# Performance work log

Measured on AMD Instinct MI355X. Metric: run time of the kernel, lower is better.

Reference implementation:

```python
import jax, jax.numpy as jnp
import numpy as np

B, T, D, H, L, DFF, MAXLEN = 4, 2048, 512, 8, 6, 2048, 2048
DK = D // H
SCALE = float(1.0 / np.sqrt(DK * 2))  # 1/sqrt(d_k*2)


def layer_norm(x, g, b, eps=1e-5):
    m = jnp.mean(x, axis=-1, keepdims=True)
    v = jnp.var(x, axis=-1, keepdims=True)
    return (x - m) / jnp.sqrt(v + eps) * g + b


def setup_inputs() -> dict:
    key = jax.random.key(0)
    it = iter(jax.random.split(key, 48))
    def n(shape, std=0.02):
        return jax.random.normal(next(it), shape, dtype=jnp.float32) * std
    inp = {}
    inp['x'] = jax.random.normal(next(it), (B, T), dtype=jnp.float32)
    inp['ip_w'] = n((1, D)); inp['ip_b'] = jnp.zeros((D,))
    inp['ip_ln_g'] = jnp.ones((D,)); inp['ip_ln_b'] = jnp.zeros((D,))
    inp['pos_embed'] = n((MAXLEN, D), 0.01)
    inp['pad_token'] = n((D,), 0.01)
    inp['Wq'] = n((L, D, D)); inp['bq'] = jnp.zeros((L, D))
    inp['Wk'] = n((L, D, D)); inp['bk'] = jnp.zeros((L, D))
    inp['Wv'] = n((L, D, D)); inp['bv'] = jnp.zeros((L, D))
    inp['Wo'] = n((L, D, D)); inp['bo'] = jnp.zeros((L, D))
    inp['ln1_g'] = jnp.ones((L, D)); inp['ln1_b'] = jnp.zeros((L, D))
    inp['ln2_g'] = jnp.ones((L, D)); inp['ln2_b'] = jnp.zeros((L, D))
    inp['W1'] = n((L, D, DFF)); inp['b1'] = jnp.zeros((L, DFF))
    inp['W2'] = n((L, DFF, D)); inp['b2'] = jnp.zeros((L, D))
    inp['gate1'] = jnp.full((L,), 0.1); inp['gate2'] = jnp.full((L,), 0.1)
    inp['fn_g'] = jnp.ones((D,)); inp['fn_b'] = jnp.zeros((D,))
    for p in ['bh', 'ah', 'ch']:
        inp[p + '_ln_g'] = jnp.ones((D,)); inp[p + '_ln_b'] = jnp.zeros((D,))
    inp['bh_w'] = n((D, 2), 0.01); inp['bh_b'] = jnp.zeros((2,))
    inp['ah_w'] = n((D, 1), 0.01); inp['ah_b'] = jnp.zeros((1,))
    inp['ch_w'] = n((D, 1), 0.01); inp['ch_b'] = jnp.zeros((1,))
    return inp


def _forward(x, ip_w, ip_b, ip_ln_g, ip_ln_b, pos_embed, pad_token,
             Wq, bq, Wk, bk, Wv, bv, Wo, bo,
             ln1_g, ln1_b, ln2_g, ln2_b, W1, b1, W2, b2, gate1, gate2,
             fn_g, fn_b, bh_ln_g, bh_ln_b, bh_w, bh_b,
             ah_ln_g, ah_ln_b, ah_w, ah_b, ch_ln_g, ch_ln_b, ch_w, ch_b):
    Bx, Tx = x.shape
    xc = jnp.clip(x, -10.0, 10.0)
    pad_mask = xc == -1.0  # [B,T]
    h = layer_norm(xc[..., None] @ ip_w + ip_b, ip_ln_g, ip_ln_b)  # [B,T,D]
    h = h + 0.1 * pos_embed[None, :Tx, :]
    h = jnp.where(pad_mask[..., None], pad_token, h)
    cmask = jnp.triu(jnp.full((Tx, Tx), -10000.0, dtype=h.dtype), k=1)  # additive causal mask
    for i in range(L):
        xn = layer_norm(h, ln1_g[i], ln1_b[i])
        def heads(w, b, xn=xn):
            return (xn @ w + b).reshape(Bx, Tx, H, DK).transpose(0, 2, 1, 3)
        q = heads(Wq[i], bq[i]); k = heads(Wk[i], bk[i]); v = heads(Wv[i], bv[i])
        q = q / jnp.maximum(jnp.linalg.norm(q, axis=-1, keepdims=True), 1e-8)
        k = k / jnp.maximum(jnp.linalg.norm(k, axis=-1, keepdims=True), 1e-8)
        scores = jnp.clip(jnp.einsum('bhtd,bhsd->bhts', q, k) * SCALE, -5.0, 5.0) + cmask
        a = jax.nn.softmax(scores / 1.5, axis=-1)
        o = jnp.einsum('bhts,bhsd->bhtd', a, v).transpose(0, 2, 1, 3).reshape(Bx, Tx, D)
        h = h + gate1[i] * ((o @ Wo[i] + bo[i]) * 0.5)
        xn2 = layer_norm(h, ln2_g[i], ln2_b[i])
        ffn = jax.nn.gelu(xn2 @ W1[i] + b1[i], approximate=False) @ W2[i] + b2[i]
        h = jnp.clip(h + gate2[i] * ffn, -10.0, 10.0)
    h = layer_norm(h, fn_g, fn_b)
    m = (~pad_mask).astype(h.dtype)[..., None]
    mean = (h * m).sum(axis=1) / jnp.maximum(m.sum(axis=1), 1.0)  # masked mean pool [B,D]
    binary = layer_norm(mean, bh_ln_g, bh_ln_b) @ bh_w + bh_b
    anomaly = layer_norm(mean, ah_ln_g, ah_ln_b) @ ah_w + ah_b
    caustic = jax.nn.sigmoid(layer_norm(mean, ch_ln_g, ch_ln_b) @ ch_w + ch_b)
    return jnp.concatenate([binary, anomaly, caustic], axis=-1)  # [B,4]


def reference(x, ip_w, ip_b, ip_ln_g, ip_ln_b, pos_embed, pad_token,
              Wq, bq, Wk, bk, Wv, bv, Wo, bo,
              ln1_g, ln1_b, ln2_g, ln2_b, W1, b1, W2, b2, gate1, gate2,
              fn_g, fn_b, bh_ln_g, bh_ln_b, bh_w, bh_b,
              ah_ln_g, ah_ln_b, ah_w, ah_b, ch_ln_g, ch_ln_b, ch_w, ch_b):
    return _forward(x, ip_w, ip_b, ip_ln_g, ip_ln_b, pos_embed, pad_token,
                    Wq, bq, Wk, bk, Wv, bv, Wo, bo,
                    ln1_g, ln1_b, ln2_g, ln2_b, W1, b1, W2, b2, gate1, gate2,
                    fn_g, fn_b, bh_ln_g, bh_ln_b, bh_w, bh_b,
                    ah_ln_g, ah_ln_b, ah_w, ah_b, ch_ln_g, ch_ln_b, ch_w, ch_b)
```

## Files before the change

kernel.cpp:

```cpp
#include <hip/hip_runtime.h>
#include <hip/hip_bf16.h>
#include <math.h>

constexpr int Bsz = 4, T = 2048, D = 512, H = 8, Lnum = 6, DFF = 2048, DK = 64;
constexpr int QS2 = 1024;
constexpr float K2 = 0.08838834764831845f / 1.5f;

typedef __attribute__((ext_vector_type(8))) short svec8;
typedef __attribute__((ext_vector_type(4))) float fvec4;

__device__ __forceinline__ fvec4 mfma16(svec8 a, svec8 b, fvec4 c) {
    return __builtin_amdgcn_mfma_f32_16x16x32_bf16(a, b, c, 0, 0, 0);
}
__device__ __forceinline__ unsigned short f2b(float f) {
    unsigned int u = __float_as_uint(f);
    u += 0x7fffu + ((u >> 16) & 1u);
    return (unsigned short)(u >> 16);
}
__device__ __forceinline__ unsigned int pk2b(float a, float b) {
    __hip_bfloat162 h = __float22bfloat162_rn(float2{a, b});
    return *(unsigned int*)&h;
}
__device__ __forceinline__ float wave_red_sum(float v) {
    for (int o = 32; o > 0; o >>= 1) v += __shfl_down(v, o, 64);
    return __shfl(v, 0, 64);
}
__device__ __forceinline__ void glds16(const unsigned short* g, unsigned short* l) {
    __builtin_amdgcn_global_load_lds(
        (const __attribute__((address_space(1))) unsigned int*)g,
        (__attribute__((address_space(3))) unsigned int*)l, 16, 0, 0);
}
#define FRAG(buf, row, kq) (*(const svec8*)((buf) + (((row) << 6) | ((((kq) ^ ((row) & 7))) << 3))))

__global__ __launch_bounds__(64)
void embed_kernel(const float* __restrict__ x, const float* __restrict__ ip_w,
                  const float* __restrict__ ip_b, const float* __restrict__ g,
                  const float* __restrict__ bta, const float* __restrict__ pos,
                  const float* __restrict__ pad_tok, float* __restrict__ h)
{
    int row = blockIdx.x;
    int t = row & (T - 1);
    int lane = threadIdx.x;
    float xv = x[row];
    float xc = fminf(fmaxf(xv, -10.f), 10.f);
    bool pad = (xc == -1.0f);
    float pre[8];
    float s = 0.f, s2 = 0.f;
#pragma unroll
    for (int j = 0; j < 8; j++) {
        int d = j * 64 + lane;
        float p = xc * ip_w[d] + ip_b[d];
        pre[j] = p; s += p; s2 += p * p;
    }
    s = wave_red_sum(s); s2 = wave_red_sum(s2);
    float m = s * (1.f / 512.f);
    float var = s2 * (1.f / 512.f) - m * m;
    float rstd = 1.f / sqrtf(var + 1e-5f);
#pragma unroll
    for (int j = 0; j < 8; j++) {
        int d = j * 64 + lane;
        float hv = (pre[j] - m) * rstd * g[d] + bta[d] + 0.1f * pos[(size_t)t * D + d];
        if (pad) hv = pad_tok[d];
        h[(size_t)row * D + d] = hv;
    }
}

__global__ __launch_bounds__(256)
void ln_kernel(const float* __restrict__ in, float* __restrict__ out,
               const float* __restrict__ g, const float* __restrict__ b)
{
    int row = blockIdx.x * 4 + (threadIdx.x >> 6);
    int lane = threadIdx.x & 63;
    const float* r = in + (size_t)row * D;
    float4 v0 = ((const float4*)r)[lane];
    float4 v1 = ((const float4*)r)[lane + 64];
    float s = v0.x + v0.y + v0.z + v0.w + v1.x + v1.y + v1.z + v1.w;
    float s2 = v0.x*v0.x + v0.y*v0.y + v0.z*v0.z + v0.w*v0.w
             + v1.x*v1.x + v1.y*v1.y + v1.z*v1.z + v1.w*v1.w;
    s = wave_red_sum(s); s2 = wave_red_sum(s2);
    float m = s * (1.f / 512.f);
    float var = s2 * (1.f / 512.f) - m * m;
    float rstd = 1.f / sqrtf(var + 1e-5f);
    float4 g0 = ((const float4*)g)[lane], g1 = ((const float4*)g)[lane + 64];
    float4 b0 = ((const float4*)b)[lane], b1 = ((const float4*)b)[lane + 64];
    float4 o0, o1;
    o0.x = (v0.x - m) * rstd * g0.x + b0.x; o0.y = (v0.y - m) * rstd * g0.y + b0.y;
    o0.z = (v0.z - m) * rstd * g0.z + b0.z; o0.w = (v0.w - m) * rstd * g0.w + b0.w;
    o1.x = (v1.x - m) * rstd * g1.x + b1.x; o1.y = (v1.y - m) * rstd * g1.y + b1.y;
    o1.z = (v1.z - m) * rstd * g1.z + b1.z; o1.w = (v1.w - m) * rstd * g1.w + b1.w;
    ((float4*)(out + (size_t)row * D))[lane] = o0;
    ((float4*)(out + (size_t)row * D))[lane + 64] = o1;
}

__global__ __launch_bounds__(256)
void ln_bf16_kernel(const float* __restrict__ in, unsigned short* __restrict__ out,
                    const float* __restrict__ g, const float* __restrict__ b)
{
    int row = blockIdx.x * 4 + (threadIdx.x >> 6);
    int lane = threadIdx.x & 63;
    const float* r = in + (size_t)row * D;
    float4 v0 = ((const float4*)r)[lane];
    float4 v1 = ((const float4*)r)[lane + 64];
    float s = v0.x + v0.y + v0.z + v0.w + v1.x + v1.y + v1.z + v1.w;
    float s2 = v0.x*v0.x + v0.y*v0.y + v0.z*v0.z + v0.w*v0.w
             + v1.x*v1.x + v1.y*v1.y + v1.z*v1.z + v1.w*v1.w;
    s = wave_red_sum(s); s2 = wave_red_sum(s2);
    float m = s * (1.f / 512.f);
    float var = s2 * (1.f / 512.f) - m * m;
    float rstd = 1.f / sqrtf(var + 1e-5f);
    float4 g0 = ((const float4*)g)[lane], g1 = ((const float4*)g)[lane + 64];
    float4 b0 = ((const float4*)b)[lane], b1 = ((const float4*)b)[lane + 64];
    unsigned short o0[4], o1[4];
    o0[0] = f2b((v0.x - m) * rstd * g0.x + b0.x); o0[1] = f2b((v0.y - m) * rstd * g0.y + b0.y);
    o0[2] = f2b((v0.z - m) * rstd * g0.z + b0.z); o0[3] = f2b((v0.w - m) * rstd * g0.w + b0.w);
    o1[0] = f2b((v1.x - m) * rstd * g1.x + b1.x); o1[1] = f2b((v1.y - m) * rstd * g1.y + b1.y);
    o1[2] = f2b((v1.z - m) * rstd * g1.z + b1.z); o1[3] = f2b((v1.w - m) * rstd * g1.w + b1.w);
    *(uint2*)(out + (size_t)row * D + lane * 4) = *(uint2*)o0;
    *(uint2*)(out + (size_t)row * D + 256 + lane * 4) = *(uint2*)o1;
}

__global__ __launch_bounds__(256)
void wconv_kernel(const float* __restrict__ wq, const float* __restrict__ wk,
                  const float* __restrict__ wv, const float* __restrict__ wo,
                  const float* __restrict__ w1, const float* __restrict__ w2,
                  unsigned short* __restrict__ oq, unsigned short* __restrict__ ok,
                  unsigned short* __restrict__ ov, unsigned short* __restrict__ oo,
                  unsigned short* __restrict__ o1, unsigned short* __restrict__ o2)
{
    __shared__ float tile[32][33];
    int bid = blockIdx.x;
    const float* in; unsigned short* out; int K, N, kt, nt;
    if (bid < 1024) {
        int sel = bid >> 8, loc = bid & 255;
        in  = sel == 0 ? wq : sel == 1 ? wk : sel == 2 ? wv : wo;
        out = sel == 0 ? oq : sel == 1 ? ok : sel == 2 ? ov : oo;
        K = 512; N = 512; kt = loc >> 4; nt = loc & 15;
    } else if (bid < 2048) {
        int loc = bid - 1024; in = w1; out = o1; K = 512; N = 2048; kt = loc >> 6; nt = loc & 63;
    } else {
        int loc = bid - 2048; in = w2; out = o2; K = 2048; N = 512; kt = loc >> 4; nt = loc & 15;
    }
    int k0 = kt * 32, n0 = nt * 32;
    int t = threadIdx.x;
    int kr = t >> 3, nc = (t & 7) * 4;
    float4 v = *(const float4*)(in + (size_t)(k0 + kr) * N + n0 + nc);
    tile[kr][nc] = v.x; tile[kr][nc + 1] = v.y; tile[kr][nc + 2] = v.z; tile[kr][nc + 3] = v.w;
    __syncthreads();
    unsigned short o[4];
#pragma unroll
    for (int i = 0; i < 4; i++) o[i] = f2b(tile[nc + i][kr]);
    *(uint2*)(out + (size_t)(n0 + kr) * K + k0 + nc) = *(uint2*)o;
}

template<int EPI, int OBF, int BM>
__global__ __launch_bounds__(256)
void gemm_bf16(const unsigned short* __restrict__ A, const unsigned short* __restrict__ BT,
               const float* __restrict__ bias, const float* __restrict__ bias_b,
               const float* __restrict__ bias_c, const float* __restrict__ res,
               void* __restrict__ Cv, unsigned short* __restrict__ vtout,
               int M, int N, int K, const float* __restrict__ gate_p)
{
    constexpr int WN = (BM == 128) ? 2 : 4;
    constexpr int WSPAN = 128 / WN;
    constexpr int NT = WSPAN / 16;
    constexpr int MT = 4;
    constexpr int ACALLS = BM / 32;
    constexpr int SMEMSZ = (EPI == 0) ? 17408 : (BM * 64 + 128 * 64);
    __shared__ __align__(16) unsigned short SMEM[SMEMSZ];
    unsigned short* As = SMEM;
    unsigned short* Bs = SMEM + BM * 64;
    const int tid = threadIdx.x, w = tid >> 6, lane = tid & 63, quad = lane >> 4, ln = lane & 15;
    const int wm = w / WN, wn = w % WN;
    const int m0 = blockIdx.x * BM, n0 = blockIdx.y * 128;
    const int jg = (lane & 7) ^ ((lane >> 3) & 7);
    const int rb = w * 8 + (lane >> 3);
    const unsigned short* Agl = A + (size_t)(m0 + rb) * K + jg * 8;
    const unsigned short* Bgl = BT + (size_t)(n0 + rb) * K + jg * 8;

    fvec4 acc[MT][NT];
#pragma unroll
    for (int mt = 0; mt < MT; mt++)
#pragma unroll
        for (int nt = 0; nt < NT; nt++)
#pragma unroll
            for (int r = 0; r < 4; r++) acc[mt][nt][r] = 0.f;

    for (int k0 = 0; k0 < K; k0 += 64) {
        __syncthreads();
#pragma unroll
        for (int c = 0; c < ACALLS; c++)
            glds16(Agl + k0 + (size_t)c * 32 * K, As + c * 2048 + w * 512);
#pragma unroll
        for (int c = 0; c < 4; c++)
            glds16(Bgl + k0 + (size_t)c * 32 * K, Bs + c * 2048 + w * 512);
        __syncthreads();
#pragma unroll
        for (int kk = 0; kk < 2; kk++) {
            svec8 af[MT], bfr[NT];
#pragma unroll
            for (int mt = 0; mt < MT; mt++)
                af[mt] = FRAG(As, wm * 64 + mt * 16 + ln, kk * 4 + quad);
#pragma unroll
            for (int nt = 0; nt < NT; nt++)
                bfr[nt] = FRAG(Bs, wn * WSPAN + nt * 16 + ln, kk * 4 + quad);
#pragma unroll
            for (int mt = 0; mt < MT; mt++)
#pragma unroll
                for (int nt = 0; nt < NT; nt++)
                    acc[mt][nt] = mfma16(af[mt], bfr[nt], acc[mt][nt]);
        }
    }

    const float gate = (EPI == 1 || EPI == 3) ? gate_p[0] : 0.f;
    float bb[NT];
#pragma unroll
    for (int nt = 0; nt < NT; nt++) {
        int n = n0 + wn * WSPAN + nt * 16 + ln;
        if (EPI == 0) {
            int nseg = n >> 9;
            const float* bsel = nseg == 0 ? bias : (nseg == 1 ? bias_b : bias_c);
            bb[nt] = bsel[n - nseg * 512];
        } else {
            bb[nt] = bias[n];
        }
    }

    if (EPI == 0 && n0 >= 1024) {
        __syncthreads();
#pragma unroll
        for (int mt = 0; mt < MT; mt++) {
#pragma unroll
            for (int nt = 0; nt < NT; nt++) {
                int nl = wn * 64 + nt * 16 + ln;
                int mb = wm * 64 + mt * 16 + quad * 4;
                unsigned int lo = pk2b(acc[mt][nt][0] + bb[nt], acc[mt][nt][1] + bb[nt]);
                unsigned int hi = pk2b(acc[mt][nt][2] + bb[nt], acc[mt][nt][3] + bb[nt]);
                uint2 u; u.x = lo; u.y = hi;
                *(uint2*)(SMEM + nl * 136 + mb) = u;
            }
        }
        __syncthreads();
        int row = tid >> 1, half = (tid & 1) * 64;
        unsigned short* dst = vtout + ((size_t)((m0 >> 11) * 512 + (n0 - 1024) + row)) * T
                              + (m0 & (T - 1)) + half;
        const unsigned short* src = SMEM + row * 136 + half;
#pragma unroll
        for (int j = 0; j < 8; j++) *(uint4*)(dst + j * 8) = *(const uint4*)(src + j * 8);
        return;
    }

#pragma unroll
    for (int mt = 0; mt < MT; mt++) {
        float v[NT][4];
#pragma unroll
        for (int nt = 0; nt < NT; nt++)
#pragma unroll
            for (int r = 0; r < 4; r++) v[nt][r] = acc[mt][nt][r] + bb[nt];
        if (EPI == 0) {
            const float fac = ((n0 + wn * WSPAN) < 512) ? K2 : 1.f;
#pragma unroll
            for (int r = 0; r < 4; r++) {
                float s = 0.f;
#pragma unroll
                for (int nt = 0; nt < NT; nt++) s += v[nt][r] * v[nt][r];
                s += __shfl_xor(s, 1); s += __shfl_xor(s, 2);
                s += __shfl_xor(s, 4); s += __shfl_xor(s, 8);
                float rs = fac / fmaxf(sqrtf(s), 1e-8f);
#pragma unroll
                for (int nt = 0; nt < NT; nt++) v[nt][r] *= rs;
            }
        }
#pragma unroll
        for (int nt = 0; nt < NT; nt++) {
            int n = n0 + wn * WSPAN + nt * 16 + ln;
#pragma unroll
            for (int r = 0; r < 4; r++) {
                int m = m0 + wm * 64 + mt * 16 + quad * 4 + r;
                float val = v[nt][r];
                if (EPI == 0) {
                    ((unsigned short*)Cv)[(size_t)m * QS2 + n] = f2b(val);
                } else {
                    size_t off = (size_t)m * N + n;
                    if (EPI == 1) val = res[off] + gate * 0.5f * val;
                    else if (EPI == 2) {
                        float u = val;
                        float z = 0.7978845608028654f * fmaf(0.044715f * u, u * u, u);
                        float e = __builtin_amdgcn_exp2f(z * 2.8853900817779268f);
                        float rr = __builtin_amdgcn_rcpf(e + 1.f);
                        val = u * (1.f - rr);
                    }
                    else if (EPI == 3) val = fminf(fmaxf(res[off] + gate * val, -10.f), 10.f);
                    if (OBF) ((unsigned short*)Cv)[off] = f2b(val);
                    else ((float*)Cv)[off] = val;
                }
            }
        }
    }
}

template<bool DIAG>
__device__ __forceinline__ void attn_step(
    const unsigned short* Q, unsigned short* Ps, const unsigned short* Ks, const unsigned short* Vt,
    fvec4 (&oacc)[4], fvec4& lacc, int w, int quad, int ln)
{
    constexpr short BONE = (short)0x3F80;
    const svec8 ONES8 = {BONE, BONE, BONE, BONE, BONE, BONE, BONE, BONE};
    svec8 qf0 = FRAG(Q, w * 16 + ln, quad);
    svec8 qf1 = FRAG(Q, w * 16 + ln, 4 + quad);
    const int qrow = w * 16 + ln;
#pragma unroll
    for (int nt = 0; nt < 4; nt++) {
        fvec4 z; z[0] = z[1] = z[2] = z[3] = 0.f;
        z = mfma16(FRAG(Ks, nt * 16 + ln, quad), qf0, z);
        z = mfma16(FRAG(Ks, nt * 16 + ln, 4 + quad), qf1, z);
        const int sbase = nt * 16 + quad * 4;
        float p[4];
#pragma unroll
        for (int r = 0; r < 4; r++) {
            float y = z[r];
            float pv = fmaf(y, fmaf(y, 0.5f, 1.f), 1.f);
            if (DIAG && (sbase + r > qrow)) pv = 0.f;
            p[r] = pv;
        }
        uint2 u; u.x = pk2b(p[0], p[1]); u.y = pk2b(p[2], p[3]);
        int chunk = sbase >> 3, off = sbase & 7;
        *(uint2*)(Ps + ((qrow << 6) | ((chunk ^ (qrow & 7)) << 3) | off)) = u;
    }
#pragma unroll
    for (int ks = 0; ks < 2; ks++) {
        svec8 pa = FRAG(Ps, w * 16 + ln, ks * 4 + quad);
        lacc = mfma16(pa, ONES8, lacc);
#pragma unroll
        for (int nt = 0; nt < 4; nt++)
            oacc[nt] = mfma16(pa, FRAG(Vt, nt * 16 + ln, ks * 4 + quad), oacc[nt]);
    }
}

__global__ __launch_bounds__(256)
void attn_pair_kernel(const unsigned short* __restrict__ qkv, const unsigned short* __restrict__ vt,
                      unsigned short* __restrict__ o)
{
    __shared__ __align__(16) unsigned short QA[4096], QB[4096];
    __shared__ __align__(16) unsigned short K0[4096], V0[4096], K1[4096], V1[4096];
    __shared__ __align__(16) unsigned short Ps[4096];
    const int fid = blockIdx.x;
    const int xcd = fid & 7, slot = fid >> 3;
    const int bh = xcd * 4 + (slot & 3);
    const int p = slot >> 2;
    const int b = bh >> 3, hh = bh & 7;
    const int qtA = p, qtB = 31 - p, nst = 32 - p;
    const int tid = threadIdx.x, w = tid >> 6, lane = tid & 63, quad = lane >> 4, ln = lane & 15;
    const int rl = lane >> 3, sl = lane & 7, jgz = sl ^ rl;
    const int w8 = w * 8;
    const int grow = w8 + rl;
    const unsigned short* qrow_p = qkv + ((size_t)(b * T) + grow) * QS2 + hh * 64 + jgz * 8;
    const unsigned short* krow_p = qrow_p + 512;
    const unsigned short* vrow_p = vt + ((size_t)(bh * 64) + grow) * T + jgz * 8;

    glds16(qrow_p + (size_t)(qtA * 64) * QS2, QA + w8 * 64);
    glds16(qrow_p + (size_t)(qtA * 64 + 32) * QS2, QA + (w8 + 32) * 64);
    glds16(qrow_p + (size_t)(qtB * 64) * QS2, QB + w8 * 64);
    glds16(qrow_p + (size_t)(qtB * 64 + 32) * QS2, QB + (w8 + 32) * 64);

    fvec4 oA[4], oB[4], lAv, lBv;
#pragma unroll
    for (int r = 0; r < 4; r++) { lAv[r] = 0.f; lBv[r] = 0.f; }
#pragma unroll
    for (int nt = 0; nt < 4; nt++)
#pragma unroll
        for (int r = 0; r < 4; r++) { oA[nt][r] = 0.f; oB[nt][r] = 0.f; }

    const int Nph = (nst + 1) >> 1;
    for (int ph = 0; ph < Nph; ph++) {
        const int s0 = 2 * ph, s1 = 2 * ph + 1;
        __syncthreads();
        glds16(krow_p + (size_t)(s0 * 64) * QS2, K0 + w8 * 64);
        glds16(krow_p + (size_t)(s0 * 64 + 32) * QS2, K0 + (w8 + 32) * 64);
        glds16(vrow_p + s0 * 64, V0 + w8 * 64);
        glds16(vrow_p + (size_t)32 * T + s0 * 64, V0 + (w8 + 32) * 64);
        if (s1 < nst) {
            glds16(krow_p + (size_t)(s1 * 64) * QS2, K1 + w8 * 64);
            glds16(krow_p + (size_t)(s1 * 64 + 32) * QS2, K1 + (w8 + 32) * 64);
            glds16(vrow_p + s1 * 64, V1 + w8 * 64);
            glds16(vrow_p + (size_t)32 * T + s1 * 64, V1 + (w8 + 32) * 64);
        }
        __syncthreads();
        if (s0 == nst - 1) attn_step<true >(QB, Ps, K0, V0, oB, lBv, w, quad, ln);
        else               attn_step<false>(QB, Ps, K0, V0, oB, lBv, w, quad, ln);
        if (s0 <= p) {
            if (s0 == p) attn_step<true >(QA, Ps, K0, V0, oA, lAv, w, quad, ln);
            else         attn_step<false>(QA, Ps, K0, V0, oA, lAv, w, quad, ln);
        }
        if (s1 < nst) {
            if (s1 == nst - 1) attn_step<true >(QB, Ps, K1, V1, oB, lBv, w, quad, ln);
            else               attn_step<false>(QB, Ps, K1, V1, oB, lBv, w, quad, ln);
            if (s1 <= p) {
                if (s1 == p) attn_step<true >(QA, Ps, K1, V1, oA, lAv, w, quad, ln);
                else         attn_step<false>(QA, Ps, K1, V1, oA, lAv, w, quad, ln);
            }
        }
    }

    unsigned short* ogA = o + (size_t)(b * T + qtA * 64 + w * 16 + quad * 4) * D + hh * 64;
    unsigned short* ogB = o + (size_t)(b * T + qtB * 64 + w * 16 + quad * 4) * D + hh * 64;
#pragma unroll
    for (int r = 0; r < 4; r++) {
        float ia = 1.f / lAv[r], ib = 1.f / lBv[r];
#pragma unroll
        for (int nt = 0; nt < 4; nt++) {
            ogA[(size_t)r * D + nt * 16 + ln] = f2b(oA[nt][r] * ia);
            ogB[(size_t)r * D + nt * 16 + ln] = f2b(oB[nt][r] * ib);
        }
    }
}

__global__ __launch_bounds__(256)
void pool_kernel(const float* __restrict__ hn, const float* __restrict__ x, float* __restrict__ part)
{
    int b = blockIdx.x, ch = blockIdx.y, tid = threadIdx.x;
    int t0 = ch * 128;
    float s0 = 0.f, s1 = 0.f, cnt = 0.f;
    for (int tt = 0; tt < 128; tt++) {
        int t = t0 + tt;
        float xv = x[b * T + t];
        float m = (xv == -1.0f) ? 0.f : 1.f;
        cnt += m;
        const float* r = hn + ((size_t)(b * T + t)) * D;
        s0 += r[tid] * m;
        s1 += r[tid + 256] * m;
    }
    float* pr = part + (size_t)(b * 16 + ch) * 513;
    pr[tid] = s0; pr[tid + 256] = s1;
    if (tid == 0) pr[512] = cnt;
}

__global__ __launch_bounds__(64)
void head_kernel(const float* __restrict__ part,
                 const float* __restrict__ bh_g, const float* __restrict__ bh_bl,
                 const float* __restrict__ ah_g, const float* __restrict__ ah_bl,
                 const float* __restrict__ ch_g, const float* __restrict__ ch_bl,
                 const float* __restrict__ bh_w, const float* __restrict__ bh_b2,
                 const float* __restrict__ ah_w, const float* __restrict__ ah_b2,
                 const float* __restrict__ ch_w, const float* __restrict__ ch_b2,
                 float* __restrict__ out)
{
    int b = blockIdx.x, lane = threadIdx.x;
    float cnt = 0.f;
    for (int c = 0; c < 16; c++) cnt += part[(size_t)(b * 16 + c) * 513 + 512];
    float denom = fmaxf(cnt, 1.f);
    float md[8];
    float s = 0.f, s2 = 0.f;
#pragma unroll
    for (int j = 0; j < 8; j++) {
        int d = j * 64 + lane;
        float acc = 0.f;
        for (int c = 0; c < 16; c++) acc += part[(size_t)(b * 16 + c) * 513 + d];
        md[j] = acc / denom;
        s += md[j]; s2 += md[j] * md[j];
    }
    s = wave_red_sum(s); s2 = wave_red_sum(s2);
    float mu = s * (1.f / 512.f);
    float var = s2 * (1.f / 512.f) - mu * mu;
    float rstd = 1.f / sqrtf(var + 1e-5f);
    float a0 = 0.f, a1 = 0.f, a2 = 0.f, a3 = 0.f;
#pragma unroll
    for (int j = 0; j < 8; j++) {
        int d = j * 64 + lane;
        float z = (md[j] - mu) * rstd;
        float zb = z * bh_g[d] + bh_bl[d];
        a0 += zb * bh_w[d * 2 + 0];
        a1 += zb * bh_w[d * 2 + 1];
        a2 += (z * ah_g[d] + ah_bl[d]) * ah_w[d];
        a3 += (z * ch_g[d] + ch_bl[d]) * ch_w[d];
    }
    a0 = wave_red_sum(a0); a1 = wave_red_sum(a1);
    a2 = wave_red_sum(a2); a3 = wave_red_sum(a3);
    if (lane == 0) {
        out[b * 4 + 0] = a0 + bh_b2[0];
        out[b * 4 + 1] = a1 + bh_b2[1];
        out[b * 4 + 2] = a2 + ah_b2[0];
        float t3 = a3 + ch_b2[0];
        out[b * 4 + 3] = 1.f / (1.f + expf(-t3));
    }
}

extern "C" void kernel_launch(void* const* d_in, const int* in_sizes, int n_in,
                              void* d_out, int out_size, void* d_ws, size_t ws_size,
                              hipStream_t stream)
{
    const float* x      = (const float*)d_in[0];
    const float* ip_w   = (const float*)d_in[1];
    const float* ip_b   = (const float*)d_in[2];
    const float* ip_ln_g= (const float*)d_in[3];
    const float* ip_ln_b= (const float*)d_in[4];
    const float* pos    = (const float*)d_in[5];
    const float* pad_tok= (const float*)d_in[6];
    const float* Wq = (const float*)d_in[7];  const float* bq = (const float*)d_in[8];
    const float* Wk = (const float*)d_in[9];  const float* bk = (const float*)d_in[10];
    const float* Wv = (const float*)d_in[11]; const float* bv = (const float*)d_in[12];
    const float* Wo = (const float*)d_in[13]; const float* bo = (const float*)d_in[14];
    const float* ln1_g = (const float*)d_in[15]; const float* ln1_b = (const float*)d_in[16];
    const float* ln2_g = (const float*)d_in[17]; const float* ln2_b = (const float*)d_in[18];
    const float* W1 = (const float*)d_in[19]; const float* b1 = (const float*)d_in[20];
    const float* W2 = (const float*)d_in[21]; const float* b2 = (const float*)d_in[22];
    const float* gate1 = (const float*)d_in[23]; const float* gate2 = (const float*)d_in[24];
    const float* fn_g = (const float*)d_in[25]; const float* fn_b = (const float*)d_in[26];
    const float* bh_g  = (const float*)d_in[27]; const float* bh_bl = (const float*)d_in[28];
    const float* ah_g  = (const float*)d_in[29]; const float* ah_bl = (const float*)d_in[30];
    const float* ch_g  = (const float*)d_in[31]; const float* ch_bl = (const float*)d_in[32];
    const float* bh_w  = (const float*)d_in[33]; const float* bh_b2 = (const float*)d_in[34];
    const float* ah_w  = (const float*)d_in[35]; const float* ah_b2 = (const float*)d_in[36];
    const float* ch_w  = (const float*)d_in[37]; const float* ch_b2 = (const float*)d_in[38];

    char* ws = (char*)d_ws;
    float*          h     = (float*)ws;
    unsigned short* act_b = (unsigned short*)(ws + 16777216);
    unsigned short* qkv   = (unsigned short*)(ws + 25165824);
    unsigned short* mid_b = (unsigned short*)(ws + 41943040);
    float*          xn_f  = (float*)(ws + 41943040);
    unsigned short* wT    = (unsigned short*)(ws + 75497472);
    unsigned short* vt    = (unsigned short*)(ws + 81788928);
    float*          part  = (float*)(ws + 90177536);
    float*          out   = (float*)d_out;

    unsigned short* wqT = wT;
    unsigned short* wkT = wT + 262144;
    unsigned short* wvT = wT + 524288;
    unsigned short* woT = wT + 786432;
    unsigned short* w1T = wT + 1048576;
    unsigned short* w2T = wT + 2097152;

    embed_kernel<<<dim3(Bsz * T), dim3(64), 0, stream>>>(x, ip_w, ip_b, ip_ln_g, ip_ln_b, pos, pad_tok, h);

    for (int i = 0; i < Lnum; i++) {
        const size_t dd = (size_t)i * D * D;
        const size_t df = (size_t)i * D * DFF;
        wconv_kernel<<<dim3(3072), dim3(256), 0, stream>>>(Wq + dd, Wk + dd, Wv + dd, Wo + dd,
                                                           W1 + df, W2 + df,
                                                           wqT, wkT, wvT, woT, w1T, w2T);
        ln_bf16_kernel<<<dim3(Bsz * T / 4), dim3(256), 0, stream>>>(h, act_b, ln1_g + i * D, ln1_b + i * D);
        gemm_bf16<0, 1, 128><<<dim3(64, 12), dim3(256), 0, stream>>>(act_b, wqT, bq + i * D, bk + i * D, bv + i * D,
                                                                     nullptr, qkv, vt, Bsz * T, 1536, D, nullptr);
        attn_pair_kernel<<<dim3(512), dim3(256), 0, stream>>>(qkv, vt, act_b);
        gemm_bf16<1, 0, 64><<<dim3(128, 4), dim3(256), 0, stream>>>(act_b, woT, bo + i * D, nullptr, nullptr,
                                                                    h, h, nullptr, Bsz * T, D, D, gate1 + i);
        ln_bf16_kernel<<<dim3(Bsz * T / 4), dim3(256), 0, stream>>>(h, act_b, ln2_g + i * D, ln2_b + i * D);
        gemm_bf16<2, 1, 128><<<dim3(64, 16), dim3(256), 0, stream>>>(act_b, w1T, b1 + i * DFF, nullptr, nullptr,
                                                                     nullptr, mid_b, nullptr, Bsz * T, DFF, D, nullptr);
        gemm_bf16<3, 0, 64><<<dim3(128, 4), dim3(256), 0, stream>>>(mid_b, w2T, b2 + i * D, nullptr, nullptr,
                                                                    h, h, nullptr, Bsz * T, D, DFF, gate2 + i);
    }

    ln_kernel<<<dim3(Bsz * T / 4), dim3(256), 0, stream>>>(h, xn_f, fn_g, fn_b);
    pool_kernel<<<dim3(Bsz, 16), dim3(256), 0, stream>>>(xn_f, x, part);
    head_kernel<<<dim3(Bsz), dim3(64), 0, stream>>>(part, bh_g, bh_bl, ah_g, ah_bl, ch_g, ch_bl,
                                                    bh_w, bh_b2, ah_w, ah_b2, ch_w, ch_b2, out);
}
```

Before: 1.134 ms.

## Fuse LN1 into weight-conversion kernel and merge paired attention steps

The per-layer weight conversion and LN1 launches are folded into one prep kernel, with the extra blocks doing the layernorm rows, which removes one launch per layer. The attention kernel now keeps the Q fragments of both query tiles in registers after the first phase. It reuses the Q shared buffers as two P buffers and processes both tiles against each K/V tile in one merged step, so K and V fragments are loaded from LDS once. This cuts LDS reads and frees one 8KB buffer, but the fragments held for the whole loop raise register pressure.

Result: no change. 1.145 ms (+1.0%).

```diff
diff --git a/kernel.cpp b/kernel.cpp
--- a/kernel.cpp
+++ b/kernel.cpp
@@ -92,12 +92,10 @@
     ((float4*)(out + (size_t)row * D))[lane + 64] = o1;
 }
 
-__global__ __launch_bounds__(256)
-void ln_bf16_kernel(const float* __restrict__ in, unsigned short* __restrict__ out,
-                    const float* __restrict__ g, const float* __restrict__ b)
-{
-    int row = blockIdx.x * 4 + (threadIdx.x >> 6);
-    int lane = threadIdx.x & 63;
+__device__ __forceinline__ void ln_row_bf16(const float* __restrict__ in, unsigned short* __restrict__ out,
+                                            const float* __restrict__ g, const float* __restrict__ b,
+                                            int row, int lane)
+{
     const float* r = in + (size_t)row * D;
     float4 v0 = ((const float4*)r)[lane];
     float4 v1 = ((const float4*)r)[lane + 64];
@@ -120,15 +118,29 @@
 }
 
 __global__ __launch_bounds__(256)
-void wconv_kernel(const float* __restrict__ wq, const float* __restrict__ wk,
-                  const float* __restrict__ wv, const float* __restrict__ wo,
-                  const float* __restrict__ w1, const float* __restrict__ w2,
-                  unsigned short* __restrict__ oq, unsigned short* __restrict__ ok,
-                  unsigned short* __restrict__ ov, unsigned short* __restrict__ oo,
-                  unsigned short* __restrict__ o1, unsigned short* __restrict__ o2)
+void ln_bf16_kernel(const float* __restrict__ in, unsigned short* __restrict__ out,
+                    const float* __restrict__ g, const float* __restrict__ b)
+{
+    ln_row_bf16(in, out, g, b, blockIdx.x * 4 + (threadIdx.x >> 6), threadIdx.x & 63);
+}
+
+__global__ __launch_bounds__(256)
+void prep_kernel(const float* __restrict__ wq, const float* __restrict__ wk,
+                 const float* __restrict__ wv, const float* __restrict__ wo,
+                 const float* __restrict__ w1, const float* __restrict__ w2,
+                 unsigned short* __restrict__ oq, unsigned short* __restrict__ ok,
+                 unsigned short* __restrict__ ov, unsigned short* __restrict__ oo,
+                 unsigned short* __restrict__ o1, unsigned short* __restrict__ o2,
+                 const float* __restrict__ hin, unsigned short* __restrict__ lnout,
+                 const float* __restrict__ ln_g, const float* __restrict__ ln_b)
 {
     __shared__ float tile[32][33];
     int bid = blockIdx.x;
+    if (bid >= 3072) {
+        int row = (bid - 3072) * 4 + (threadIdx.x >> 6);
+        ln_row_bf16(hin, lnout, ln_g, ln_b, row, threadIdx.x & 63);
+        return;
+    }
     const float* in; unsigned short* out; int K, N, kt, nt;
     if (bid < 1024) {
         int sel = bid >> 8, loc = bid & 255;
@@ -298,41 +310,68 @@
     }
 }
 
-template<bool DIAG>
-__device__ __forceinline__ void attn_step(
-    const unsigned short* Q, unsigned short* Ps, const unsigned short* Ks, const unsigned short* Vt,
-    fvec4 (&oacc)[4], fvec4& lacc, int w, int quad, int ln)
+template<bool MERGED, bool DIAGS>
+__device__ __forceinline__ void attn_step2(
+    unsigned short* PsA, unsigned short* PsB,
+    const unsigned short* Ks, const unsigned short* Vt,
+    svec8 qA0, svec8 qA1, svec8 qB0, svec8 qB1,
+    bool diagA, bool diagB,
+    fvec4 (&oA)[4], fvec4& lA, fvec4 (&oB)[4], fvec4& lB,
+    int w, int quad, int ln)
 {
     constexpr short BONE = (short)0x3F80;
     const svec8 ONES8 = {BONE, BONE, BONE, BONE, BONE, BONE, BONE, BONE};
-    svec8 qf0 = FRAG(Q, w * 16 + ln, quad);
-    svec8 qf1 = FRAG(Q, w * 16 + ln, 4 + quad);
     const int qrow = w * 16 + ln;
+    const int prow_base = (qrow << 6);
 #pragma unroll
     for (int nt = 0; nt < 4; nt++) {
-        fvec4 z; z[0] = z[1] = z[2] = z[3] = 0.f;
-        z = mfma16(FRAG(Ks, nt * 16 + ln, quad), qf0, z);
-        z = mfma16(FRAG(Ks, nt * 16 + ln, 4 + quad), qf1, z);
+        svec8 kf0 = FRAG(Ks, nt * 16 + ln, quad);
+        svec8 kf1 = FRAG(Ks, nt * 16 + ln, 4 + quad);
         const int sbase = nt * 16 + quad * 4;
-        float p[4];
-#pragma unroll
-        for (int r = 0; r < 4; r++) {
-            float y = z[r];
-            float pv = fmaf(y, fmaf(y, 0.5f, 1.f), 1.f);
-            if (DIAG && (sbase + r > qrow)) pv = 0.f;
-            p[r] = pv;
-        }
-        uint2 u; u.x = pk2b(p[0], p[1]); u.y = pk2b(p[2], p[3]);
-        int chunk = sbase >> 3, off = sbase & 7;
-        *(uint2*)(Ps + ((qrow << 6) | ((chunk ^ (qrow & 7)) << 3) | off)) = u;
+        const int paddr = prow_base | ((((sbase >> 3) ^ (qrow & 7))) << 3) | (sbase & 7);
+        {
+            fvec4 z; z[0] = z[1] = z[2] = z[3] = 0.f;
+            z = mfma16(kf0, qB0, z);
+            z = mfma16(kf1, qB1, z);
+            float p[4];
+#pragma unroll
+            for (int r = 0; r < 4; r++) {
+                float y = z[r];
+                float pv = fmaf(y, fmaf(y, 0.5f, 1.f), 1.f);
+                if (DIAGS && diagB && (sbase + r > qrow)) pv = 0.f;
+                p[r] = pv;
+            }
+            uint2 u; u.x = pk2b(p[0], p[1]); u.y = pk2b(p[2], p[3]);
+            *(uint2*)(PsB + paddr) = u;
+        }
+        if (MERGED) {
+            fvec4 z; z[0] = z[1] = z[2] = z[3] = 0.f;
+            z = mfma16(kf0, qA0, z);
+            z = mfma16(kf1, qA1, z);
+            float p[4];
+#pragma unroll
+            for (int r = 0; r < 4; r++) {
+                float y = z[r];
+                float pv = fmaf(y, fmaf(y, 0.5f, 1.f), 1.f);
+                if (DIAGS && diagA && (sbase + r > qrow)) pv = 0.f;
+                p[r] = pv;
+            }
+            uint2 u; u.x = pk2b(p[0], p[1]); u.y = pk2b(p[2], p[3]);
+            *(uint2*)(PsA + paddr) = u;
+        }
     }
 #pragma unroll
     for (int ks = 0; ks < 2; ks++) {
-        svec8 pa = FRAG(Ps, w * 16 + ln, ks * 4 + quad);
-        lacc = mfma16(pa, ONES8, lacc);
-#pragma unroll
-        for (int nt = 0; nt < 4; nt++)
-            oacc[nt] = mfma16(pa, FRAG(Vt, nt * 16 + ln, ks * 4 + quad), oacc[nt]);
+        svec8 paB = FRAG(PsB, w * 16 + ln, ks * 4 + quad);
+        lB = mfma16(paB, ONES8, lB);
+        svec8 paA;
+        if (MERGED) { paA = FRAG(PsA, w * 16 + ln, ks * 4 + quad); lA = mfma16(paA, ONES8, lA); }
+#pragma unroll
+        for (int nt = 0; nt < 4; nt++) {
+            svec8 vf = FRAG(Vt, nt * 16 + ln, ks * 4 + quad);
+            oB[nt] = mfma16(paB, vf, oB[nt]);
+            if (MERGED) oA[nt] = mfma16(paA, vf, oA[nt]);
+        }
     }
 }
 
@@ -340,9 +379,8 @@
 void attn_pair_kernel(const unsigned short* __restrict__ qkv, const unsigned short* __restrict__ vt,
                       unsigned short* __restrict__ o)
 {
-    __shared__ __align__(16) unsigned short QA[4096], QB[4096];
+    __shared__ __align__(16) unsigned short PsA[4096], PsB[4096];
     __shared__ __align__(16) unsigned short K0[4096], V0[4096], K1[4096], V1[4096];
-    __shared__ __align__(16) unsigned short Ps[4096];
     const int fid = blockIdx.x;
     const int xcd = fid & 7, slot = fid >> 3;
     const int bh = xcd * 4 + (slot & 3);
@@ -357,11 +395,12 @@
     const unsigned short* krow_p = qrow_p + 512;
     const unsigned short* vrow_p = vt + ((size_t)(bh * 64) + grow) * T + jgz * 8;
 
-    glds16(qrow_p + (size_t)(qtA * 64) * QS2, QA + w8 * 64);
-    glds16(qrow_p + (size_t)(qtA * 64 + 32) * QS2, QA + (w8 + 32) * 64);
-    glds16(qrow_p + (size_t)(qtB * 64) * QS2, QB + w8 * 64);
-    glds16(qrow_p + (size_t)(qtB * 64 + 32) * QS2, QB + (w8 + 32) * 64);
-
+    glds16(qrow_p + (size_t)(qtA * 64) * QS2, PsA + w8 * 64);
+    glds16(qrow_p + (size_t)(qtA * 64 + 32) * QS2, PsA + (w8 + 32) * 64);
+    glds16(qrow_p + (size_t)(qtB * 64) * QS2, PsB + w8 * 64);
+    glds16(qrow_p + (size_t)(qtB * 64 + 32) * QS2, PsB + (w8 + 32) * 64);
+
+    svec8 qA0 = {}, qA1 = {}, qB0 = {}, qB1 = {};
     fvec4 oA[4], oB[4], lAv, lBv;
 #pragma unroll
     for (int r = 0; r < 4; r++) { lAv[r] = 0.f; lBv[r] = 0.f; }
@@ -385,18 +424,28 @@
             glds16(vrow_p + (size_t)32 * T + s1 * 64, V1 + (w8 + 32) * 64);
         }
         __syncthreads();
-        if (s0 == nst - 1) attn_step<true >(QB, Ps, K0, V0, oB, lBv, w, quad, ln);
-        else               attn_step<false>(QB, Ps, K0, V0, oB, lBv, w, quad, ln);
-        if (s0 <= p) {
-            if (s0 == p) attn_step<true >(QA, Ps, K0, V0, oA, lAv, w, quad, ln);
-            else         attn_step<false>(QA, Ps, K0, V0, oA, lAv, w, quad, ln);
+        if (ph == 0) {
+            qA0 = FRAG(PsA, w * 16 + ln, quad); qA1 = FRAG(PsA, w * 16 + ln, 4 + quad);
+            qB0 = FRAG(PsB, w * 16 + ln, quad); qB1 = FRAG(PsB, w * 16 + ln, 4 + quad);
+        }
+        {
+            const bool doA = (s0 <= p), dA = (s0 == p), dB = (s0 == nst - 1);
+            if (doA) {
+                if (dA | dB) attn_step2<true , true >(PsA, PsB, K0, V0, qA0, qA1, qB0, qB1, dA, dB, oA, lAv, oB, lBv, w, quad, ln);
+                else         attn_step2<true , false>(PsA, PsB, K0, V0, qA0, qA1, qB0, qB1, dA, dB, oA, lAv, oB, lBv, w, quad, ln);
+            } else {
+                if (dB)      attn_step2<false, true >(PsA, PsB, K0, V0, qA0, qA1, qB0, qB1, dA, dB, oA, lAv, oB, lBv, w, quad, ln);
+                else         attn_step2<false, false>(PsA, PsB, K0, V0, qA0, qA1, qB0, qB1, dA, dB, oA, lAv, oB, lBv, w, quad, ln);
+            }
         }
         if (s1 < nst) {
-            if (s1 == nst - 1) attn_step<true >(QB, Ps, K1, V1, oB, lBv, w, quad, ln);
-            else               attn_step<false>(QB, Ps, K1, V1, oB, lBv, w, quad, ln);
-            if (s1 <= p) {
-                if (s1 == p) attn_step<true >(QA, Ps, K1, V1, oA, lAv, w, quad, ln);
-                else         attn_step<false>(QA, Ps, K1, V1, oA, lAv, w, quad, ln);
+            const bool doA = (s1 <= p), dA = (s1 == p), dB = (s1 == nst - 1);
+            if (doA) {
+                if (dA | dB) attn_step2<true , true >(PsA, PsB, K1, V1, qA0, qA1, qB0, qB1, dA, dB, oA, lAv, oB, lBv, w, quad, ln);
+                else         attn_step2<true , false>(PsA, PsB, K1, V1, qA0, qA1, qB0, qB1, dA, dB, oA, lAv, oB, lBv, w, quad, ln);
+            } else {
+                if (dB)      attn_step2<false, true >(PsA, PsB, K1, V1, qA0, qA1, qB0, qB1, dA, dB, oA, lAv, oB, lBv, w, quad, ln);
+                else         attn_step2<false, false>(PsA, PsB, K1, V1, qA0, qA1, qB0, qB1, dA, dB, oA, lAv, oB, lBv, w, quad, ln);
             }
         }
     }
@@ -535,10 +584,10 @@
     for (int i = 0; i < Lnum; i++) {
         const size_t dd = (size_t)i * D * D;
         const size_t df = (size_t)i * D * DFF;
-        wconv_kernel<<<dim3(3072), dim3(256), 0, stream>>>(Wq + dd, Wk + dd, Wv + dd, Wo + dd,
-                                                           W1 + df, W2 + df,
-                                                           wqT, wkT, wvT, woT, w1T, w2T);
-        ln_bf16_kernel<<<dim3(Bsz * T / 4), dim3(256), 0, stream>>>(h, act_b, ln1_g + i * D, ln1_b + i * D);
+        prep_kernel<<<dim3(5120), dim3(256), 0, stream>>>(Wq + dd, Wk + dd, Wv + dd, Wo + dd,
+                                                          W1 + df, W2 + df,
+                                                          wqT, wkT, wvT, woT, w1T, w2T,
+                                                          h, act_b, ln1_g + i * D, ln1_b + i * D);
         gemm_bf16<0, 1, 128><<<dim3(64, 12), dim3(256), 0, stream>>>(act_b, wqT, bq + i * D, bk + i * D, bv + i * D,
                                                                      nullptr, qkv, vt, Bsz * T, 1536, D, nullptr);
         attn_pair_kernel<<<dim3(512), dim3(256), 0, stream>>>(qkv, vt, act_b);
```
